# Performance work log

Hardware: AMD Instinct MI355X
Metric: run time of the kernel (lower is better)

The kernel has to match this reference:

```python
import jax, jax.numpy as jnp
import numpy as np

T, B, F = 128, 128, 1024
ALPHA_BASE, LAMBDA_BASE = 0.97, 0.95
THETA_BASE, BETA_THETA = 0.1, 0.01
RHO, GATE_ALPHA = 0.25, 5.0        # gate_cfg rho_B/rho_C, alpha
NUDGE, PHASE_SCALE = 0.1, 0.02     # gate_cfg additive_nudge, ei_cfg phase_corr_scale
MIX_AMP, MIX_NOV, MIX_INST = 1.0, 0.5, 0.5


def _adaptive_percentile_threshold(score, rho, alpha):
    # keep top-rho fraction per row: tau = (1-rho)-quantile, soft sigmoid gate
    tau = jnp.quantile(score, 1.0 - rho, axis=-1, keepdims=True)
    return jax.nn.sigmoid(alpha * (score - tau)), tau


def setup_inputs() -> dict:
    key = jax.random.key(0)
    k0, k1, k2, k3 = jax.random.split(key, 4)
    return {
        "in_re": jax.random.normal(k0, (T, B, F), jnp.float32),
        "in_im": jax.random.normal(k1, (T, B, F), jnp.float32),
        "r_re": 0.05 * jax.random.normal(k2, (F,), jnp.float32),
        "r_im": 0.05 * jax.random.normal(k3, (F,), jnp.float32),
        "alpha_map": jnp.zeros((F,), jnp.float32),
        "lambda_map": jnp.zeros((F,), jnp.float32),
    }


def reference(in_re, in_im, r_re, r_im, alpha_map, lambda_map):
    sg = jax.lax.stop_gradient
    alpha = jnp.clip(ALPHA_BASE + 0.05 * jnp.tanh(alpha_map), 0.9, 0.995)  # [F]
    lam = jnp.clip(LAMBDA_BASE + 0.05 * jnp.tanh(lambda_map), 0.9, 0.995)  # [F]
    r_conj = jnp.conj(r_re + 1j * r_im)                                    # [F] c64
    theta_base = jnp.full((F,), THETA_BASE, jnp.float32)
    in_field = (in_re + 1j * in_im).astype(jnp.complex64)                  # [T,B,F]

    carry0 = dict(
        X=jnp.zeros((B, F), jnp.complex64),
        sA=jnp.zeros((B, F), jnp.float32),
        sB=jnp.zeros((B, F), jnp.float32),
        sC=jnp.zeros((B, F), jnp.float32),
        theta=theta_base,
        mu=jnp.zeros((F,), jnp.float32),
        var=jnp.full((F,), 0.01, jnp.float32),
        ema_unit=jnp.zeros((F,), jnp.complex64),
        b_usage=jnp.zeros((F,), jnp.float32),
        c_usage=jnp.zeros((F,), jnp.float32),
    )

    def step(c, u):
        X_mid = alpha * c["X"] + u                       # [B,F] c64
        amp = jnp.abs(X_mid)
        unit = jnp.exp(1j * jnp.angle(X_mid))            # unit phase
        # EMA stats (torch.no_grad -> stop_gradient)
        mu = sg(0.9 * c["mu"] + 0.1 * amp.mean(0))
        var = sg(0.9 * c["var"] + 0.1 * ((amp - mu[None]) ** 2).mean(0))
        ema_unit = sg(0.9 * c["ema_unit"] + 0.1 * unit.mean(0))
        plv = jnp.abs(ema_unit)                          # [F]
        zscore = (amp - mu[None]) / (jnp.sqrt(var)[None] + 1e-3)
        instab = (1.0 - plv)[None]
        score = MIX_AMP * amp + MIX_NOV * jnp.abs(zscore) + MIX_INST * instab
        gB, _ = _adaptive_percentile_threshold(score, RHO, GATE_ALPHA)
        gC, _ = _adaptive_percentile_threshold(-score, RHO, GATE_ALPHA)
        XB = X_mid * gB
        XC = X_mid * gC
        sA = lam * c["sA"] + jnp.real(X_mid * r_conj)
        sB = lam * c["sB"] + jnp.real(XB * r_conj)
        sC = lam * c["sC"] + jnp.real(XC * r_conj)
        evA = (sA >= c["theta"]).astype(jnp.float32)
        evB = (sB >= c["theta"]).astype(jnp.float32)
        evC = (sC >= c["theta"]).astype(jnp.float32)
        # threshold homeostasis (no_grad)
        theta = c["theta"] + 0.01 * evB.mean(0) - 0.01 * evC.mean(0)
        theta = jnp.clip(theta - BETA_THETA * (theta - theta_base), 0.01, 10.0)
        # reentry_mode='full': phase correction + additive nudge
        corr = (evB.mean(0) > 0).astype(jnp.float32)[None]  # [1,F]
        XA = X_mid * jnp.exp(1j * PHASE_SCALE * corr)
        XA = XA + NUDGE * (XB * corr)
        b_usage = 0.99 * c["b_usage"] + 0.01 * evB.mean(0)
        c_usage = 0.99 * c["c_usage"] + 0.01 * evC.mean(0)
        new = dict(X=XA, sA=sA, sB=sB, sC=sC, theta=theta, mu=mu, var=var,
                   ema_unit=ema_unit, b_usage=b_usage, c_usage=c_usage)
        return new, sA

    _, sA_seq = jax.lax.scan(step, carry0, in_field)
    return sA_seq  # [T,B,F]
```

## Files before the change

### kernel.cpp

```cpp
#include <hip/hip_runtime.h>
#include <math.h>


#define T_STEPS 128
#define B_DIM   128
#define F_DIM   1024
#define NWG     128
#define NTH     256
#define BF      (B_DIM * F_DIM)

typedef unsigned long long ull;

__device__ __forceinline__ ull ld64(const ull* p) {
  return __hip_atomic_load(p, __ATOMIC_RELAXED, __HIP_MEMORY_SCOPE_AGENT);
}
__device__ __forceinline__ void st64(ull* p, ull v) {
  __hip_atomic_store(p, v, __ATOMIC_RELAXED, __HIP_MEMORY_SCOPE_AGENT);
}

extern "C" __global__ void __launch_bounds__(NTH)
ResonatorABC_82094004896068_kernel(
    const float* __restrict__ in_re, const float* __restrict__ in_im,
    const float* __restrict__ r_re_p, const float* __restrict__ r_im_p,
    const float* __restrict__ alpha_map, const float* __restrict__ lambda_map,
    float* __restrict__ out, ull* __restrict__ ws)
{
  const int tid  = threadIdx.x;
  const int wg   = blockIdx.x;
  const int fl   = tid & 7;
  const int rg   = tid >> 3;
  const int f    = (wg << 3) + fl;
  const int wid  = tid >> 6;
  const int lane = tid & 63;

  ull* score64 = ws;
  ull* taubox  = ws + BF;

  __shared__ __align__(16) float pamp[4][8][4];
  __shared__ __align__(16) float pev[4][8][2];
  __shared__ __align__(16) unsigned h[1024];
  __shared__ unsigned wsum[4];
  __shared__ unsigned win[2];
  __shared__ unsigned tbin[4], tbase[4], tcnt[4];
  __shared__ unsigned lcnt[4];
  __shared__ unsigned lists[4][256];
  __shared__ unsigned resv[4], resf[4];
  __shared__ unsigned rmm[2];
  __shared__ unsigned t2[3];
  __shared__ float tauLds[256];

  const float af = fminf(fmaxf(0.97f + 0.05f * tanhf(alpha_map[f]), 0.90f), 0.995f);
  const float lf = fminf(fmaxf(0.95f + 0.05f * tanhf(lambda_map[f]), 0.90f), 0.995f);
  const float rr = r_re_p[f];
  const float ri = r_im_p[f];
  const float c002 = cosf(0.02f);
  const float s002 = sinf(0.02f);

  float X_re[4] = {0.f,0.f,0.f,0.f}, X_im[4] = {0.f,0.f,0.f,0.f};
  float sA[4] = {0.f,0.f,0.f,0.f}, sB[4] = {0.f,0.f,0.f,0.f}, sC[4] = {0.f,0.f,0.f,0.f};
  float mu = 0.f, var = 0.01f, theta = 0.1f, ema_re = 0.f, ema_im = 0.f;

  int idx[4];
  float ur[4], ui[4];
  #pragma unroll
  for (int k = 0; k < 4; ++k) {
    idx[k] = (rg + 32 * k) * F_DIM + f;
    ur[k] = in_re[idx[k]];
    ui[k] = in_im[idx[k]];
  }

  const unsigned KR[4] = {255u, 256u, 767u, 768u};

  if (tid == 0) { win[0] = 0x3E000000u; win[1] = 0x42000000u; }
  __syncthreads();

  for (int t = 0; t < T_STEPS; ++t) {
    const ull want = (ull)(t + 1);

    *(uint4*)&h[4 * tid] = make_uint4(0u, 0u, 0u, 0u);

    float Xm_re[4], Xm_im[4], proj[4], amp[4], score[4];
    float a0 = 0.f, a1 = 0.f, a2 = 0.f, a3 = 0.f;
    #pragma unroll
    for (int k = 0; k < 4; ++k) {
      Xm_re[k] = af * X_re[k] + ur[k];
      Xm_im[k] = af * X_im[k] + ui[k];
      float amp2 = Xm_re[k] * Xm_re[k] + Xm_im[k] * Xm_im[k];
      amp[k] = sqrtf(amp2);
      float invamp = (amp[k] > 0.f) ? (1.0f / amp[k]) : 0.f;
      float un_re = (amp[k] > 0.f) ? (Xm_re[k] * invamp) : 1.0f;
      float un_im = Xm_im[k] * invamp;
      proj[k] = Xm_re[k] * rr + Xm_im[k] * ri;
      sA[k] = lf * sA[k] + proj[k];
      out[t * BF + idx[k]] = sA[k];
      a0 += amp[k]; a1 += amp2; a2 += un_re; a3 += un_im;
    }
    #pragma unroll
    for (int m = 8; m < 64; m <<= 1) {
      a0 += __shfl_xor(a0, m);
      a1 += __shfl_xor(a1, m);
      a2 += __shfl_xor(a2, m);
      a3 += __shfl_xor(a3, m);
    }
    if (lane < 8) { *(float4*)&pamp[wid][lane][0] = make_float4(a0, a1, a2, a3); }
    __syncthreads();
    float4 P0 = *(const float4*)&pamp[0][fl][0];
    float4 P1 = *(const float4*)&pamp[1][fl][0];
    float4 P2 = *(const float4*)&pamp[2][fl][0];
    float4 P3 = *(const float4*)&pamp[3][fl][0];
    float S0 = P0.x + P1.x + P2.x + P3.x;
    float S1 = P0.y + P1.y + P2.y + P3.y;
    float S2 = P0.z + P1.z + P2.z + P3.z;
    float S3 = P0.w + P1.w + P2.w + P3.w;
    float m1 = S0 * 0.0078125f;
    float m2 = S1 * 0.0078125f;
    mu = 0.9f * mu + 0.1f * m1;
    float vm = m2 - 2.f * mu * m1 + mu * mu;
    vm = fmaxf(vm, 0.f);
    var = 0.9f * var + 0.1f * vm;
    ema_re = 0.9f * ema_re + 0.1f * (S2 * 0.0078125f);
    ema_im = 0.9f * ema_im + 0.1f * (S3 * 0.0078125f);
    float plv = sqrtf(ema_re * ema_re + ema_im * ema_im);
    float sden = sqrtf(var) + 1e-3f;
    #pragma unroll
    for (int k = 0; k < 4; ++k) {
      float zs = (amp[k] - mu) / sden;
      score[k] = amp[k] + 0.5f * fabsf(zs) + 0.5f * (1.0f - plv);
      st64(&score64[idx[k]], (want << 32) | (ull)__float_as_uint(score[k]));
    }

    float ur_n[4] = {0.f,0.f,0.f,0.f}, ui_n[4] = {0.f,0.f,0.f,0.f};
    if (t + 1 < T_STEPS) {
      #pragma unroll
      for (int k = 0; k < 4; ++k) {
        ur_n[k] = in_re[(t + 1) * BF + idx[k]];
        ui_n[k] = in_im[(t + 1) * BF + idx[k]];
      }
    }

    const unsigned wlo = win[0], whi = win[1];
    const unsigned range = whi - wlo + 1u;
    int shift = (range <= 1024u) ? 0 : (22 - __clz(range - 1u));
    if (shift < 0) shift = 0;
    const unsigned maxbin = (range - 1u) >> shift;

    unsigned uval[4], bin[4];
    {
      const ull* sp0 = &score64[wg * F_DIM + tid];
      ull v[4]; bool ok[4] = {false, false, false, false};
      int remaining = 4;
      while (remaining) {
        #pragma unroll
        for (int k = 0; k < 4; ++k) if (!ok[k]) v[k] = ld64(sp0 + 256 * k);
        #pragma unroll
        for (int k = 0; k < 4; ++k) {
          if (!ok[k] && (v[k] >> 32) == want) { ok[k] = true; uval[k] = (unsigned)v[k]; --remaining; }
        }
        if (remaining) __builtin_amdgcn_s_sleep(4);
      }
    }
    #pragma unroll
    for (int k = 0; k < 4; ++k) {
      unsigned uc = min(max(uval[k], wlo), whi);
      bin[k] = (uc - wlo) >> shift;
      atomicAdd(&h[bin[k]], 1u);
    }
    if (tid >= 64 && tid < 68) { lcnt[tid - 64] = 0u; resf[tid - 64] = 0u; }
    __syncthreads();

    if (wid == 0) {
      uint4 q0 = *(const uint4*)&h[16 * lane +  0];
      uint4 q1 = *(const uint4*)&h[16 * lane +  4];
      uint4 q2 = *(const uint4*)&h[16 * lane +  8];
      uint4 q3 = *(const uint4*)&h[16 * lane + 12];
      unsigned c16[16] = {q0.x,q0.y,q0.z,q0.w, q1.x,q1.y,q1.z,q1.w,
                          q2.x,q2.y,q2.z,q2.w, q3.x,q3.y,q3.z,q3.w};
      unsigned s16 = 0;
      #pragma unroll
      for (int i = 0; i < 16; ++i) s16 += c16[i];
      unsigned incl = s16;
      #pragma unroll
      for (int d = 1; d < 64; d <<= 1) {
        unsigned vv = __shfl_up(incl, d);
        if (lane >= d) incl += vv;
      }
      unsigned excl = incl - s16;
      unsigned bacc = excl;
      #pragma unroll
      for (int i = 0; i < 16; ++i) {
        unsigned c = c16[i];
        if (c) {
          #pragma unroll
          for (int r = 0; r < 4; ++r) {
            if (bacc <= KR[r] && KR[r] < bacc + c) {
              tbin[r] = 16 * lane + i; tbase[r] = bacc; tcnt[r] = c;
            }
          }
        }
        bacc += c;
      }
      int fi = 16, li = -1;
      #pragma unroll
      for (int i = 0; i < 16; ++i) if (c16[i]) { if (fi == 16) fi = i; li = i; }
      unsigned long long occ = __ballot(s16 > 0);
      int flane = __builtin_ctzll(occ);
      int llane = 63 - __builtin_clzll(occ);
      int fin = __shfl(fi, flane);
      int lin = __shfl(li, llane);
      if (lane == 0) {
        unsigned first_bin = (unsigned)(16 * flane + fin);
        unsigned last_bin  = (unsigned)(16 * llane + lin);
        unsigned nlo, nhi;
        if (first_bin == 0u) {
          unsigned w4 = range >> 2;
          nlo = (wlo > w4) ? (wlo - w4) : 0u;
        } else {
          nlo = wlo + ((first_bin - 1u) << shift);
        }
        if (last_bin >= maxbin) {
          ull tt = (ull)whi + (ull)(range >> 2);
          nhi = (tt > 0x7F7FFFFFull) ? 0x7F7FFFFFu : (unsigned)tt;
        } else {
          ull tt = (ull)wlo + (((ull)(last_bin + 2u)) << shift) - 1ull;
          nhi = (tt > 0x7F7FFFFFull) ? 0x7F7FFFFFu : (unsigned)tt;
        }
        win[0] = nlo; win[1] = nhi;
      }
    }
    __syncthreads();

    {
      unsigned b0 = tbin[0], b1 = tbin[1], b2 = tbin[2], b3 = tbin[3];
      #pragma unroll
      for (int k = 0; k < 4; ++k) {
        unsigned bk = bin[k], uv = uval[k];
        if (bk == b0) { unsigned s = atomicAdd(&lcnt[0], 1u); if (s < 256u) lists[0][s] = uv; }
        else if (bk == b1 && b1 != b0) { unsigned s = atomicAdd(&lcnt[1], 1u); if (s < 256u) lists[1][s] = uv; }
        else if (bk == b2 && b2 != b1) { unsigned s = atomicAdd(&lcnt[2], 1u); if (s < 256u) lists[2][s] = uv; }
        else if (bk == b3 && b3 != b2) { unsigned s = atomicAdd(&lcnt[3], 1u); if (s < 256u) lists[3][s] = uv; }
      }
    }
    __syncthreads();

    {
      const int j = wid;
      int src = j;
      while (src > 0 && tbin[src - 1] == tbin[j]) --src;
      unsigned c = tcnt[j];
      if (c <= 256u) {
        unsigned kk = KR[j] - tbase[j];
        for (int bi = 0; bi < (int)c; bi += 64) {
          int i = bi + lane;
          if (i < (int)c) {
            unsigned e = lists[src][i];
            unsigned r = 0;
            for (int q = 0; q < (int)c; ++q) {
              unsigned x = lists[src][q];
              r += (x < e || (x == e && q < i)) ? 1u : 0u;
            }
            if (r == kk) { resv[j] = e; resf[j] = 1u; }
          }
        }
      }
    }
    __syncthreads();

    for (int j = 0; j < 4; ++j) {
      if (resf[j]) continue;
      bool inj[4];
      #pragma unroll
      for (int k = 0; k < 4; ++k) inj[k] = (bin[k] == tbin[j]);
      unsigned krem = KR[j] - tbase[j];
      for (int iter = 0; iter < 40; ++iter) {
        if (tid == 0) { rmm[0] = 0xFFFFFFFFu; rmm[1] = 0u; }
        __syncthreads();
        #pragma unroll
        for (int k = 0; k < 4; ++k)
          if (inj[k]) { atomicMin(&rmm[0], uval[k]); atomicMax(&rmm[1], uval[k]); }
        __syncthreads();
        unsigned wlo2 = rmm[0], whi2 = rmm[1];
        if (wlo2 == whi2) { if (tid == 0) { resv[j] = wlo2; resf[j] = 1u; } __syncthreads(); break; }
        *(uint4*)&h[4 * tid] = make_uint4(0u, 0u, 0u, 0u);
        __syncthreads();
        ull rng2 = (ull)whi2 - (ull)wlo2 + 1ull;
        ull inv2 = (1ull << 40) / rng2;
        unsigned nb[4];
        #pragma unroll
        for (int k = 0; k < 4; ++k) {
          nb[k] = inj[k] ? (unsigned)((((ull)(uval[k] - wlo2)) * inv2) >> 30) : 0u;
          if (inj[k]) atomicAdd(&h[nb[k]], 1u);
        }
        __syncthreads();
        uint4 hc2 = *(const uint4*)&h[4 * tid];
        unsigned s42 = hc2.x + hc2.y + hc2.z + hc2.w;
        unsigned incl2 = s42;
        #pragma unroll
        for (int d = 1; d < 64; d <<= 1) {
          unsigned vv = __shfl_up(incl2, d);
          if (lane >= d) incl2 += vv;
        }
        if (lane == 63) wsum[wid] = incl2;
        if (tid == 0) lcnt[0] = 0u;
        __syncthreads();
        unsigned woff2 = 0u;
        for (int w = 0; w < 4; ++w) if (w < wid) woff2 += wsum[w];
        unsigned gexcl2 = woff2 + incl2 - s42;
        unsigned cv2[4] = {hc2.x, hc2.y, hc2.z, hc2.w};
        unsigned bb2[4];
        bb2[0] = gexcl2; bb2[1] = bb2[0] + cv2[0]; bb2[2] = bb2[1] + cv2[1]; bb2[3] = bb2[2] + cv2[2];
        #pragma unroll
        for (int i = 0; i < 4; ++i) {
          if (cv2[i] > 0u && bb2[i] <= krem && krem < bb2[i] + cv2[i]) {
            t2[0] = 4 * tid + i; t2[1] = bb2[i]; t2[2] = cv2[i];
          }
        }
        __syncthreads();
        unsigned nbin = t2[0], nbase = t2[1], ncnt = t2[2];
        bool newin[4];
        #pragma unroll
        for (int k = 0; k < 4; ++k) newin[k] = inj[k] && (nb[k] == nbin);
        if (ncnt <= 256u) {
          #pragma unroll
          for (int k = 0; k < 4; ++k)
            if (newin[k]) { unsigned s = atomicAdd(&lcnt[0], 1u); if (s < 256u) lists[0][s] = uval[k]; }
          __syncthreads();
          if (wid == 0) {
            unsigned kk2 = krem - nbase;
            for (int bi = 0; bi < (int)ncnt; bi += 64) {
              int i = bi + lane;
              if (i < (int)ncnt) {
                unsigned e = lists[0][i];
                unsigned r = 0;
                for (int q = 0; q < (int)ncnt; ++q) {
                  unsigned x = lists[0][q];
                  r += (x < e || (x == e && q < i)) ? 1u : 0u;
                }
                if (r == kk2) { resv[j] = e; resf[j] = 1u; }
              }
            }
          }
          __syncthreads();
          break;
        }
        #pragma unroll
        for (int k = 0; k < 4; ++k) inj[k] = newin[k];
        krem -= nbase;
      }
    }

    {
      float s255 = __uint_as_float(resv[0]);
      float s256 = __uint_as_float(resv[1]);
      float s767 = __uint_as_float(resv[2]);
      float s768 = __uint_as_float(resv[3]);
      float tb = 0.75f * s767 + 0.25f * s768;
      float tc = -(0.75f * s256 + 0.25f * s255);
      int c = tid & 127;
      ull w = (tid < 128)
            ? ((want << 32) | (ull)__float_as_uint(tb))
            : ((want << 32) | (ull)__float_as_uint(tc));
      int slot = (tid < 128) ? wg : (128 + wg);
      st64(&taubox[(ull)c * 256 + slot], w);
    }

    {
      const ull* src = &taubox[(ull)wg * 256 + tid];
      ull v2 = ld64(src);
      while ((v2 >> 32) != want) { __builtin_amdgcn_s_sleep(2); v2 = ld64(src); }
      tauLds[tid] = __uint_as_float((unsigned)v2);
    }
    __syncthreads();

    float gB[4];
    float e0 = 0.f, e1 = 0.f;
    #pragma unroll
    for (int k = 0; k < 4; ++k) {
      float tb = tauLds[rg + 32 * k];
      float tc = tauLds[128 + rg + 32 * k];
      float sc = score[k];
      gB[k] = 1.0f / (1.0f + expf(-5.0f * (sc - tb)));
      float gC = 1.0f / (1.0f + expf(-5.0f * (-sc - tc)));
      sB[k] = lf * sB[k] + proj[k] * gB[k];
      sC[k] = lf * sC[k] + proj[k] * gC;
      e0 += (sB[k] >= theta) ? 1.0f : 0.0f;
      e1 += (sC[k] >= theta) ? 1.0f : 0.0f;
    }
    #pragma unroll
    for (int m = 8; m < 64; m <<= 1) {
      e0 += __shfl_xor(e0, m);
      e1 += __shfl_xor(e1, m);
    }
    if (lane < 8) { pev[wid][lane][0] = e0; pev[wid][lane][1] = e1; }
    __syncthreads();
    float2 E0 = *(const float2*)&pev[0][fl][0];
    float2 E1 = *(const float2*)&pev[1][fl][0];
    float2 E2 = *(const float2*)&pev[2][fl][0];
    float2 E3 = *(const float2*)&pev[3][fl][0];
    float cB = E0.x + E1.x + E2.x + E3.x;
    float cC = E0.y + E1.y + E2.y + E3.y;
    float th1 = theta + 0.01f * (cB * 0.0078125f) - 0.01f * (cC * 0.0078125f);
    theta = fminf(fmaxf(th1 - 0.01f * (th1 - 0.1f), 0.01f), 10.0f);
    bool corr = (cB > 0.f);
    #pragma unroll
    for (int k = 0; k < 4; ++k) {
      float fac_re = corr ? (c002 + 0.1f * gB[k]) : 1.0f;
      float fac_im = corr ? s002 : 0.0f;
      X_re[k] = Xm_re[k] * fac_re - Xm_im[k] * fac_im;
      X_im[k] = Xm_re[k] * fac_im + Xm_im[k] * fac_re;
      ur[k] = ur_n[k]; ui[k] = ui_n[k];
    }
  }
}

extern "C" void kernel_launch(void* const* d_in, const int* in_sizes, int n_in,
                              void* d_out, int out_size, void* d_ws, size_t ws_size,
                              hipStream_t stream) {
  const float* in_re = (const float*)d_in[0];
  const float* in_im = (const float*)d_in[1];
  const float* r_re  = (const float*)d_in[2];
  const float* r_im  = (const float*)d_in[3];
  const float* amap  = (const float*)d_in[4];
  const float* lmap  = (const float*)d_in[5];
  float* out = (float*)d_out;
  ull* ws = (ull*)d_ws;
  hipMemsetAsync(d_ws, 0, (size_t)(BF + 128 * 256) * 8, stream);
  hipLaunchKernelGGL(ResonatorABC_82094004896068_kernel,
                     dim3(NWG), dim3(NTH), 0, stream,
                     in_re, in_im, r_re, r_im, amap, lmap, out, ws);
}
```

Baseline: 1.314 ms.

## Use per-row min/max histogram window and compact tau exchange via global slots

The adaptive histogram window carried across timesteps is replaced by a fresh per-row min/max reduction over wave shuffles, so the first histogram pass is scaled to the actual score range. The all-equal case now short-circuits. The tau exchange changes from a 128x256 transposed mailbox, with each thread writing one slot, to two 128-entry arrays written by a single thread per workgroup. Every thread then polls the tau values it needs directly, which drops the LDS staging, one barrier and the sleep calls in the spin loops. The risks are more contention from the polling on a small set of shared cache lines, and a possibly coarser first-pass histogram that pushes more work into refinement iterations.

```diff
diff --git a/kernel.cpp b/kernel.cpp
--- a/kernel.cpp
+++ b/kernel.cpp
@@ -34,20 +34,20 @@
   const int lane = tid & 63;
 
   ull* score64 = ws;
-  ull* taubox  = ws + BF;
+  ull* tauB64  = ws + BF;
+  ull* tauC64  = ws + BF + 128;
 
   __shared__ __align__(16) float pamp[4][8][4];
   __shared__ __align__(16) float pev[4][8][2];
   __shared__ __align__(16) unsigned h[1024];
   __shared__ unsigned wsum[4];
-  __shared__ unsigned win[2];
+  __shared__ unsigned mmw[4][2];
   __shared__ unsigned tbin[4], tbase[4], tcnt[4];
   __shared__ unsigned lcnt[4];
   __shared__ unsigned lists[4][256];
   __shared__ unsigned resv[4], resf[4];
   __shared__ unsigned rmm[2];
   __shared__ unsigned t2[3];
-  __shared__ float tauLds[256];
 
   const float af = fminf(fmaxf(0.97f + 0.05f * tanhf(alpha_map[f]), 0.90f), 0.995f);
   const float lf = fminf(fmaxf(0.95f + 0.05f * tanhf(lambda_map[f]), 0.90f), 0.995f);
@@ -70,9 +70,6 @@
   }
 
   const unsigned KR[4] = {255u, 256u, 767u, 768u};
-
-  if (tid == 0) { win[0] = 0x3E000000u; win[1] = 0x42000000u; }
-  __syncthreads();
 
   for (int t = 0; t < T_STEPS; ++t) {
     const ull want = (ull)(t + 1);
@@ -138,12 +135,6 @@
       }
     }
 
-    const unsigned wlo = win[0], whi = win[1];
-    const unsigned range = whi - wlo + 1u;
-    int shift = (range <= 1024u) ? 0 : (22 - __clz(range - 1u));
-    if (shift < 0) shift = 0;
-    const unsigned maxbin = (range - 1u) >> shift;
-
     unsigned uval[4], bin[4];
     {
       const ull* sp0 = &score64[wg * F_DIM + tid];
@@ -156,230 +147,223 @@
         for (int k = 0; k < 4; ++k) {
           if (!ok[k] && (v[k] >> 32) == want) { ok[k] = true; uval[k] = (unsigned)v[k]; --remaining; }
         }
-        if (remaining) __builtin_amdgcn_s_sleep(4);
-      }
-    }
-    #pragma unroll
-    for (int k = 0; k < 4; ++k) {
-      unsigned uc = min(max(uval[k], wlo), whi);
-      bin[k] = (uc - wlo) >> shift;
-      atomicAdd(&h[bin[k]], 1u);
-    }
-    if (tid >= 64 && tid < 68) { lcnt[tid - 64] = 0u; resf[tid - 64] = 0u; }
+      }
+    }
+    unsigned umin = min(min(uval[0], uval[1]), min(uval[2], uval[3]));
+    unsigned umax = max(max(uval[0], uval[1]), max(uval[2], uval[3]));
+    #pragma unroll
+    for (int m = 1; m < 64; m <<= 1) {
+      umin = min(umin, (unsigned)__shfl_xor((int)umin, m));
+      umax = max(umax, (unsigned)__shfl_xor((int)umax, m));
+    }
+    if (lane == 0) { mmw[wid][0] = umin; mmw[wid][1] = umax; }
+    if (tid < 4) { lcnt[tid] = 0u; resf[tid] = 0u; }
     __syncthreads();
-
-    if (wid == 0) {
-      uint4 q0 = *(const uint4*)&h[16 * lane +  0];
-      uint4 q1 = *(const uint4*)&h[16 * lane +  4];
-      uint4 q2 = *(const uint4*)&h[16 * lane +  8];
-      uint4 q3 = *(const uint4*)&h[16 * lane + 12];
-      unsigned c16[16] = {q0.x,q0.y,q0.z,q0.w, q1.x,q1.y,q1.z,q1.w,
-                          q2.x,q2.y,q2.z,q2.w, q3.x,q3.y,q3.z,q3.w};
-      unsigned s16 = 0;
-      #pragma unroll
-      for (int i = 0; i < 16; ++i) s16 += c16[i];
-      unsigned incl = s16;
-      #pragma unroll
-      for (int d = 1; d < 64; d <<= 1) {
-        unsigned vv = __shfl_up(incl, d);
-        if (lane >= d) incl += vv;
-      }
-      unsigned excl = incl - s16;
-      unsigned bacc = excl;
-      #pragma unroll
-      for (int i = 0; i < 16; ++i) {
-        unsigned c = c16[i];
-        if (c) {
-          #pragma unroll
-          for (int r = 0; r < 4; ++r) {
-            if (bacc <= KR[r] && KR[r] < bacc + c) {
-              tbin[r] = 16 * lane + i; tbase[r] = bacc; tcnt[r] = c;
-            }
-          }
-        }
-        bacc += c;
-      }
-      int fi = 16, li = -1;
-      #pragma unroll
-      for (int i = 0; i < 16; ++i) if (c16[i]) { if (fi == 16) fi = i; li = i; }
-      unsigned long long occ = __ballot(s16 > 0);
-      int flane = __builtin_ctzll(occ);
-      int llane = 63 - __builtin_clzll(occ);
-      int fin = __shfl(fi, flane);
-      int lin = __shfl(li, llane);
-      if (lane == 0) {
-        unsigned first_bin = (unsigned)(16 * flane + fin);
-        unsigned last_bin  = (unsigned)(16 * llane + lin);
-        unsigned nlo, nhi;
-        if (first_bin == 0u) {
-          unsigned w4 = range >> 2;
-          nlo = (wlo > w4) ? (wlo - w4) : 0u;
-        } else {
-          nlo = wlo + ((first_bin - 1u) << shift);
-        }
-        if (last_bin >= maxbin) {
-          ull tt = (ull)whi + (ull)(range >> 2);
-          nhi = (tt > 0x7F7FFFFFull) ? 0x7F7FFFFFu : (unsigned)tt;
-        } else {
-          ull tt = (ull)wlo + (((ull)(last_bin + 2u)) << shift) - 1ull;
-          nhi = (tt > 0x7F7FFFFFull) ? 0x7F7FFFFFu : (unsigned)tt;
-        }
-        win[0] = nlo; win[1] = nhi;
-      }
-    }
-    __syncthreads();
-
-    {
-      unsigned b0 = tbin[0], b1 = tbin[1], b2 = tbin[2], b3 = tbin[3];
+    unsigned lo = min(min(mmw[0][0], mmw[1][0]), min(mmw[2][0], mmw[3][0]));
+    unsigned hi = max(max(mmw[0][1], mmw[1][1]), max(mmw[2][1], mmw[3][1]));
+
+    if (lo != hi) {
+      ull rng = (ull)hi - (ull)lo + 1ull;
+      ull inv = (1ull << 40) / rng;
       #pragma unroll
       for (int k = 0; k < 4; ++k) {
-        unsigned bk = bin[k], uv = uval[k];
-        if (bk == b0) { unsigned s = atomicAdd(&lcnt[0], 1u); if (s < 256u) lists[0][s] = uv; }
-        else if (bk == b1 && b1 != b0) { unsigned s = atomicAdd(&lcnt[1], 1u); if (s < 256u) lists[1][s] = uv; }
-        else if (bk == b2 && b2 != b1) { unsigned s = atomicAdd(&lcnt[2], 1u); if (s < 256u) lists[2][s] = uv; }
-        else if (bk == b3 && b3 != b2) { unsigned s = atomicAdd(&lcnt[3], 1u); if (s < 256u) lists[3][s] = uv; }
-      }
-    }
-    __syncthreads();
-
-    {
-      const int j = wid;
-      int src = j;
-      while (src > 0 && tbin[src - 1] == tbin[j]) --src;
-      unsigned c = tcnt[j];
-      if (c <= 256u) {
-        unsigned kk = KR[j] - tbase[j];
-        for (int bi = 0; bi < (int)c; bi += 64) {
-          int i = bi + lane;
-          if (i < (int)c) {
-            unsigned e = lists[src][i];
-            unsigned r = 0;
-            for (int q = 0; q < (int)c; ++q) {
-              unsigned x = lists[src][q];
-              r += (x < e || (x == e && q < i)) ? 1u : 0u;
-            }
-            if (r == kk) { resv[j] = e; resf[j] = 1u; }
-          }
-        }
-      }
-    }
-    __syncthreads();
-
-    for (int j = 0; j < 4; ++j) {
-      if (resf[j]) continue;
-      bool inj[4];
-      #pragma unroll
-      for (int k = 0; k < 4; ++k) inj[k] = (bin[k] == tbin[j]);
-      unsigned krem = KR[j] - tbase[j];
-      for (int iter = 0; iter < 40; ++iter) {
-        if (tid == 0) { rmm[0] = 0xFFFFFFFFu; rmm[1] = 0u; }
-        __syncthreads();
-        #pragma unroll
-        for (int k = 0; k < 4; ++k)
-          if (inj[k]) { atomicMin(&rmm[0], uval[k]); atomicMax(&rmm[1], uval[k]); }
-        __syncthreads();
-        unsigned wlo2 = rmm[0], whi2 = rmm[1];
-        if (wlo2 == whi2) { if (tid == 0) { resv[j] = wlo2; resf[j] = 1u; } __syncthreads(); break; }
-        *(uint4*)&h[4 * tid] = make_uint4(0u, 0u, 0u, 0u);
-        __syncthreads();
-        ull rng2 = (ull)whi2 - (ull)wlo2 + 1ull;
-        ull inv2 = (1ull << 40) / rng2;
-        unsigned nb[4];
-        #pragma unroll
-        for (int k = 0; k < 4; ++k) {
-          nb[k] = inj[k] ? (unsigned)((((ull)(uval[k] - wlo2)) * inv2) >> 30) : 0u;
-          if (inj[k]) atomicAdd(&h[nb[k]], 1u);
-        }
-        __syncthreads();
-        uint4 hc2 = *(const uint4*)&h[4 * tid];
-        unsigned s42 = hc2.x + hc2.y + hc2.z + hc2.w;
-        unsigned incl2 = s42;
+        bin[k] = (unsigned)((((ull)(uval[k] - lo)) * inv) >> 30);
+        atomicAdd(&h[bin[k]], 1u);
+      }
+      __syncthreads();
+
+      if (wid == 0) {
+        uint4 q0 = *(const uint4*)&h[16 * lane +  0];
+        uint4 q1 = *(const uint4*)&h[16 * lane +  4];
+        uint4 q2 = *(const uint4*)&h[16 * lane +  8];
+        uint4 q3 = *(const uint4*)&h[16 * lane + 12];
+        unsigned c16[16] = {q0.x,q0.y,q0.z,q0.w, q1.x,q1.y,q1.z,q1.w,
+                            q2.x,q2.y,q2.z,q2.w, q3.x,q3.y,q3.z,q3.w};
+        unsigned s16 = 0;
+        #pragma unroll
+        for (int i = 0; i < 16; ++i) s16 += c16[i];
+        unsigned incl = s16;
         #pragma unroll
         for (int d = 1; d < 64; d <<= 1) {
-          unsigned vv = __shfl_up(incl2, d);
-          if (lane >= d) incl2 += vv;
-        }
-        if (lane == 63) wsum[wid] = incl2;
-        if (tid == 0) lcnt[0] = 0u;
-        __syncthreads();
-        unsigned woff2 = 0u;
-        for (int w = 0; w < 4; ++w) if (w < wid) woff2 += wsum[w];
-        unsigned gexcl2 = woff2 + incl2 - s42;
-        unsigned cv2[4] = {hc2.x, hc2.y, hc2.z, hc2.w};
-        unsigned bb2[4];
-        bb2[0] = gexcl2; bb2[1] = bb2[0] + cv2[0]; bb2[2] = bb2[1] + cv2[1]; bb2[3] = bb2[2] + cv2[2];
-        #pragma unroll
-        for (int i = 0; i < 4; ++i) {
-          if (cv2[i] > 0u && bb2[i] <= krem && krem < bb2[i] + cv2[i]) {
-            t2[0] = 4 * tid + i; t2[1] = bb2[i]; t2[2] = cv2[i];
-          }
-        }
-        __syncthreads();
-        unsigned nbin = t2[0], nbase = t2[1], ncnt = t2[2];
-        bool newin[4];
-        #pragma unroll
-        for (int k = 0; k < 4; ++k) newin[k] = inj[k] && (nb[k] == nbin);
-        if (ncnt <= 256u) {
-          #pragma unroll
-          for (int k = 0; k < 4; ++k)
-            if (newin[k]) { unsigned s = atomicAdd(&lcnt[0], 1u); if (s < 256u) lists[0][s] = uval[k]; }
-          __syncthreads();
-          if (wid == 0) {
-            unsigned kk2 = krem - nbase;
-            for (int bi = 0; bi < (int)ncnt; bi += 64) {
-              int i = bi + lane;
-              if (i < (int)ncnt) {
-                unsigned e = lists[0][i];
-                unsigned r = 0;
-                for (int q = 0; q < (int)ncnt; ++q) {
-                  unsigned x = lists[0][q];
-                  r += (x < e || (x == e && q < i)) ? 1u : 0u;
-                }
-                if (r == kk2) { resv[j] = e; resf[j] = 1u; }
+          unsigned vv = __shfl_up(incl, d);
+          if (lane >= d) incl += vv;
+        }
+        unsigned bacc = incl - s16;
+        #pragma unroll
+        for (int i = 0; i < 16; ++i) {
+          unsigned c = c16[i];
+          if (c) {
+            #pragma unroll
+            for (int r = 0; r < 4; ++r) {
+              if (bacc <= KR[r] && KR[r] < bacc + c) {
+                tbin[r] = 16 * lane + i; tbase[r] = bacc; tcnt[r] = c;
               }
             }
           }
-          __syncthreads();
-          break;
-        }
-        #pragma unroll
-        for (int k = 0; k < 4; ++k) inj[k] = newin[k];
-        krem -= nbase;
-      }
-    }
-
-    {
+          bacc += c;
+        }
+      }
+      __syncthreads();
+
+      {
+        unsigned b0 = tbin[0], b1 = tbin[1], b2 = tbin[2], b3 = tbin[3];
+        #pragma unroll
+        for (int k = 0; k < 4; ++k) {
+          unsigned bk = bin[k], uv = uval[k];
+          if (bk == b0) { unsigned s = atomicAdd(&lcnt[0], 1u); if (s < 256u) lists[0][s] = uv; }
+          else if (bk == b1 && b1 != b0) { unsigned s = atomicAdd(&lcnt[1], 1u); if (s < 256u) lists[1][s] = uv; }
+          else if (bk == b2 && b2 != b1) { unsigned s = atomicAdd(&lcnt[2], 1u); if (s < 256u) lists[2][s] = uv; }
+          else if (bk == b3 && b3 != b2) { unsigned s = atomicAdd(&lcnt[3], 1u); if (s < 256u) lists[3][s] = uv; }
+        }
+      }
+      __syncthreads();
+
+      {
+        const int j = wid;
+        int src = j;
+        while (src > 0 && tbin[src - 1] == tbin[j]) --src;
+        unsigned c = tcnt[j];
+        if (c <= 256u) {
+          unsigned kk = KR[j] - tbase[j];
+          for (int bi = 0; bi < (int)c; bi += 64) {
+            int i = bi + lane;
+            if (i < (int)c) {
+              unsigned e = lists[src][i];
+              unsigned r = 0;
+              for (int q = 0; q < (int)c; ++q) {
+                unsigned x = lists[src][q];
+                r += (x < e || (x == e && q < i)) ? 1u : 0u;
+              }
+              if (r == kk) { resv[j] = e; resf[j] = 1u; }
+            }
+          }
+        }
+      }
+      __syncthreads();
+
+      for (int j = 0; j < 4; ++j) {
+        if (resf[j]) continue;
+        bool inj[4];
+        #pragma unroll
+        for (int k = 0; k < 4; ++k) inj[k] = (bin[k] == tbin[j]);
+        unsigned krem = KR[j] - tbase[j];
+        for (int iter = 0; iter < 40; ++iter) {
+          if (tid == 0) { rmm[0] = 0xFFFFFFFFu; rmm[1] = 0u; }
+          __syncthreads();
+          #pragma unroll
+          for (int k = 0; k < 4; ++k)
+            if (inj[k]) { atomicMin(&rmm[0], uval[k]); atomicMax(&rmm[1], uval[k]); }
+          __syncthreads();
+          unsigned wlo = rmm[0], whi = rmm[1];
+          if (wlo == whi) { if (tid == 0) { resv[j] = wlo; resf[j] = 1u; } __syncthreads(); break; }
+          *(uint4*)&h[4 * tid] = make_uint4(0u, 0u, 0u, 0u);
+          __syncthreads();
+          ull rng2 = (ull)whi - (ull)wlo + 1ull;
+          ull inv2 = (1ull << 40) / rng2;
+          unsigned nb[4];
+          #pragma unroll
+          for (int k = 0; k < 4; ++k) {
+            nb[k] = inj[k] ? (unsigned)((((ull)(uval[k] - wlo)) * inv2) >> 30) : 0u;
+            if (inj[k]) atomicAdd(&h[nb[k]], 1u);
+          }
+          __syncthreads();
+          uint4 hc2 = *(const uint4*)&h[4 * tid];
+          unsigned s42 = hc2.x + hc2.y + hc2.z + hc2.w;
+          unsigned incl2 = s42;
+          #pragma unroll
+          for (int d = 1; d < 64; d <<= 1) {
+            unsigned vv = __shfl_up(incl2, d);
+            if (lane >= d) incl2 += vv;
+          }
+          if (lane == 63) wsum[wid] = incl2;
+          if (tid == 0) lcnt[0] = 0u;
+          __syncthreads();
+          unsigned woff2 = 0u;
+          for (int w = 0; w < 4; ++w) if (w < wid) woff2 += wsum[w];
+          unsigned gexcl2 = woff2 + incl2 - s42;
+          unsigned cv2[4] = {hc2.x, hc2.y, hc2.z, hc2.w};
+          unsigned bb2[4];
+          bb2[0] = gexcl2; bb2[1] = bb2[0] + cv2[0]; bb2[2] = bb2[1] + cv2[1]; bb2[3] = bb2[2] + cv2[2];
+          #pragma unroll
+          for (int i = 0; i < 4; ++i) {
+            if (cv2[i] > 0u && bb2[i] <= krem && krem < bb2[i] + cv2[i]) {
+              t2[0] = 4 * tid + i; t2[1] = bb2[i]; t2[2] = cv2[i];
+            }
+          }
+          __syncthreads();
+          unsigned nbin = t2[0], nbase = t2[1], ncnt = t2[2];
+          bool newin[4];
+          #pragma unroll
+          for (int k = 0; k < 4; ++k) newin[k] = inj[k] && (nb[k] == nbin);
+          if (ncnt <= 256u) {
+            #pragma unroll
+            for (int k = 0; k < 4; ++k)
+              if (newin[k]) { unsigned s = atomicAdd(&lcnt[0], 1u); if (s < 256u) lists[0][s] = uval[k]; }
+            __syncthreads();
+            if (wid == 0) {
+              unsigned kk2 = krem - nbase;
+              for (int bi = 0; bi < (int)ncnt; bi += 64) {
+                int i = bi + lane;
+                if (i < (int)ncnt) {
+                  unsigned e = lists[0][i];
+                  unsigned r = 0;
+                  for (int q = 0; q < (int)ncnt; ++q) {
+                    unsigned x = lists[0][q];
+                    r += (x < e || (x == e && q < i)) ? 1u : 0u;
+                  }
+                  if (r == kk2) { resv[j] = e; resf[j] = 1u; }
+                }
+              }
+            }
+            __syncthreads();
+            break;
+          }
+          #pragma unroll
+          for (int k = 0; k < 4; ++k) inj[k] = newin[k];
+          krem -= nbase;
+        }
+      }
+    } else {
+      if (tid < 4) { resv[tid] = lo; resf[tid] = 1u; }
+      __syncthreads();
+    }
+
+    if (tid == 0) {
       float s255 = __uint_as_float(resv[0]);
       float s256 = __uint_as_float(resv[1]);
       float s767 = __uint_as_float(resv[2]);
       float s768 = __uint_as_float(resv[3]);
       float tb = 0.75f * s767 + 0.25f * s768;
       float tc = -(0.75f * s256 + 0.25f * s255);
-      int c = tid & 127;
-      ull w = (tid < 128)
-            ? ((want << 32) | (ull)__float_as_uint(tb))
-            : ((want << 32) | (ull)__float_as_uint(tc));
-      int slot = (tid < 128) ? wg : (128 + wg);
-      st64(&taubox[(ull)c * 256 + slot], w);
-    }
-
+      st64(&tauB64[wg], (want << 32) | (ull)__float_as_uint(tb));
+      st64(&tauC64[wg], (want << 32) | (ull)__float_as_uint(tc));
+    }
+
+    float tbv[4], tcv[4];
     {
-      const ull* src = &taubox[(ull)wg * 256 + tid];
-      ull v2 = ld64(src);
-      while ((v2 >> 32) != want) { __builtin_amdgcn_s_sleep(2); v2 = ld64(src); }
-      tauLds[tid] = __uint_as_float((unsigned)v2);
-    }
-    __syncthreads();
+      ull vb[4], vc[4]; bool okb[4] = {false,false,false,false}, okc[4] = {false,false,false,false};
+      int remaining = 8;
+      while (remaining) {
+        #pragma unroll
+        for (int k = 0; k < 4; ++k) {
+          if (!okb[k]) vb[k] = ld64(&tauB64[rg + 32 * k]);
+          if (!okc[k]) vc[k] = ld64(&tauC64[rg + 32 * k]);
+        }
+        #pragma unroll
+        for (int k = 0; k < 4; ++k) {
+          if (!okb[k] && (vb[k] >> 32) == want) { okb[k] = true; tbv[k] = __uint_as_float((unsigned)vb[k]); --remaining; }
+          if (!okc[k] && (vc[k] >> 32) == want) { okc[k] = true; tcv[k] = __uint_as_float((unsigned)vc[k]); --remaining; }
+        }
+      }
+    }
 
     float gB[4];
     float e0 = 0.f, e1 = 0.f;
     #pragma unroll
     for (int k = 0; k < 4; ++k) {
-      float tb = tauLds[rg + 32 * k];
-      float tc = tauLds[128 + rg + 32 * k];
       float sc = score[k];
-      gB[k] = 1.0f / (1.0f + expf(-5.0f * (sc - tb)));
-      float gC = 1.0f / (1.0f + expf(-5.0f * (-sc - tc)));
+      gB[k] = 1.0f / (1.0f + expf(-5.0f * (sc - tbv[k])));
+      float gC = 1.0f / (1.0f + expf(-5.0f * (-sc - tcv[k])));
       sB[k] = lf * sB[k] + proj[k] * gB[k];
       sC[k] = lf * sC[k] + proj[k] * gC;
       e0 += (sB[k] >= theta) ? 1.0f : 0.0f;
@@ -423,7 +407,7 @@
   const float* lmap  = (const float*)d_in[5];
   float* out = (float*)d_out;
   ull* ws = (ull*)d_ws;
-  hipMemsetAsync(d_ws, 0, (size_t)(BF + 128 * 256) * 8, stream);
+  hipMemsetAsync(d_ws, 0, (size_t)(BF + 256) * 8, stream);
   hipLaunchKernelGGL(ResonatorABC_82094004896068_kernel,
                      dim3(NWG), dim3(NTH), 0, stream,
                      in_re, in_im, r_re, r_im, amap, lmap, out, ws);
```

Measured after the change: 1.362 ms. +3.7%, slower.
